# Kernel optimization log

Hardware: AMD Instinct MI355X
Metric: run time of the kernel (lower is better)

The kernel has to match this reference:

```python
import jax, jax.numpy as jnp
import numpy as np

NUM_STATION = 20
NUM_HEADS = 8
INPUT_DIM = 128
KEY_DIM = 16          # = val_dim = embed_dim // num_heads
EMBED_DIM = 128
NORM = 1.0 / np.sqrt(KEY_DIM).astype(np.float32)


def setup_inputs() -> dict:
    key = jax.random.key(0)
    ks = jax.random.split(key, 10)
    B, N, D = 32, 1024, INPUT_DIM
    q = jax.random.normal(ks[0], (B, N, D), jnp.float32)
    h = jax.random.normal(ks[1], (B, N, D), jnp.float32)
    stdv_k = 1.0 / np.sqrt(KEY_DIM)      # torch init: uniform(-1/sqrt(last_dim), ...)
    stdv_e = 1.0 / np.sqrt(EMBED_DIM)
    def U(k, shape, s):
        return jax.random.uniform(k, shape, jnp.float32, -s, s)
    pshape = (NUM_HEADS, INPUT_DIM, KEY_DIM)
    return {
        "q": q,
        "h": h,
        "W_query_custom": U(ks[2], pshape, stdv_k),
        "W_query_custom_1": U(ks[3], pshape, stdv_k),
        "W_key_custom": U(ks[4], pshape, stdv_k),
        "W_val_custom": U(ks[5], pshape, stdv_k),
        "W_query_charge_1": U(ks[6], pshape, stdv_k),
        "W_key_charge": U(ks[7], pshape, stdv_k),
        "W_val_charge": U(ks[8], pshape, stdv_k),
        "W_out": U(ks[9], (NUM_HEADS, KEY_DIM, EMBED_DIM), stdv_e),
    }


def reference(q, h, W_query_custom, W_query_custom_1, W_key_custom, W_val_custom,
              W_query_charge_1, W_key_charge, W_val_charge, W_out):
    S = NUM_STATION + 1                      # depot + stations
    h_st, h_tk = h[:, :S], h[:, S:]          # [B,S,D], [B,T,D]
    q_st, q_tk = q[:, :S], q[:, S:]

    proj = lambda x, W: jnp.einsum('bnd,hdk->hbnk', x, W)

    K_c = proj(h_tk, W_key_custom)           # [H,B,T,K]
    V_c = proj(h_tk, W_val_custom)
    K_s = proj(h_st, W_key_charge)           # [H,B,S,K]
    V_s = proj(h_st, W_val_charge)

    # task -> task attention (queries via W_query_custom_1)
    Q_tt = proj(q_tk, W_query_custom_1)
    A_tt = jax.nn.softmax(NORM * jnp.einsum('hbqk,hbtk->hbqt', Q_tt, K_c), axis=-1)
    heads_t = jnp.einsum('hbqt,hbtk->hbqk', A_tt, V_c)

    # task -> station attention (queries via W_query_custom)
    Q_ts = proj(q_tk, W_query_custom)
    A_ts = jax.nn.softmax(NORM * jnp.einsum('hbqk,hbsk->hbqs', Q_ts, K_s), axis=-1)
    heads_t = heads_t + jnp.einsum('hbqs,hbsk->hbqk', A_ts, V_s)

    # station -> task attention (queries via W_query_charge_1)
    Q_st = proj(q_st, W_query_charge_1)
    A_st = jax.nn.softmax(NORM * jnp.einsum('hbqk,hbtk->hbqt', Q_st, K_c), axis=-1)
    heads_s = jnp.einsum('hbqt,hbtk->hbqk', A_st, V_c)

    heads = jnp.concatenate([heads_s, heads_t], axis=2)   # [H,B,N,K]
    out = jnp.einsum('hbnk,hke->bne', heads, W_out)        # [B,N,E]
    return out
```

## Files before the change

### kernel.cpp

```cpp
#include <hip/hip_runtime.h>

typedef __bf16 bf16x8 __attribute__((ext_vector_type(8)));
typedef float f32x4 __attribute__((ext_vector_type(4)));
typedef float f32x16 __attribute__((ext_vector_type(16)));
typedef unsigned int uint32;
typedef unsigned short u16;

#define NST 21
#define TOK 1003
#define SCL 0.3606737602222409f

union U4B { uint4 u; bf16x8 b; };

__device__ __forceinline__ uint32 pkbf(float a, float b) {
  uint32 ua = __float_as_uint(a), ub = __float_as_uint(b);
  ua += 0x7fffu + ((ua >> 16) & 1u);
  ub += 0x7fffu + ((ub >> 16) & 1u);
  return (ua >> 16) | (ub & 0xffff0000u);
}
__device__ __forceinline__ u16 bf1(float a) {
  uint32 u = __float_as_uint(a);
  u += 0x7fffu + ((u >> 16) & 1u);
  return (u16)(u >> 16);
}
__device__ __forceinline__ uint32 pkperm(float lo, float hi) {
  return __builtin_amdgcn_perm(__float_as_uint(hi), __float_as_uint(lo), 0x07060302u);
}
__device__ __forceinline__ void plswap(uint32& a, uint32& b) {
#if __has_builtin(__builtin_amdgcn_permlane32_swap)
  typedef unsigned int uu2 __attribute__((ext_vector_type(2)));
  uu2 r = __builtin_amdgcn_permlane32_swap(a, b, false, false);
  a = r.x; b = r.y;
#else
  asm volatile("v_permlane32_swap_b32 %0, %1" : "+v"(a), "+v"(b));
#endif
}

__global__ __launch_bounds__(256) void prep(
    const float* __restrict__ q, const float* __restrict__ hx,
    const float* __restrict__ W0, const float* __restrict__ W1,
    const float* __restrict__ W2, const float* __restrict__ W3,
    const float* __restrict__ W4, const float* __restrict__ Wqst,
    const float* __restrict__ Wks, const float* __restrict__ Wvs,
    u16* __restrict__ WtAll, u16* __restrict__ Qm,
    u16* __restrict__ Ks, u16* __restrict__ Vs) {
  int bid = blockIdx.x, tid = threadIdx.x;
  __shared__ float xq2[2][128], xh2[2][128];
  if (bid < 40) {
    int w = bid >> 3, seg = bid & 7;
    const float* W = (w == 0) ? W0 : (w == 1) ? W1 : (w == 2) ? W2
                     : (w == 3) ? W3 : W4;
    u16* dst = WtAll + w * 16384;
#pragma unroll
    for (int it = 0; it < 8; ++it) {
      int i = seg * 2048 + it * 256 + tid;
      int inner = i & 127, outer = i >> 7;
      float v;
      if (w < 4) {
        int h = outer >> 4, k = outer & 15;
        v = W[h * 2048 + inner * 16 + k];
      } else {
        v = W[inner * 128 + outer];
      }
      dst[outer * 128 + inner] = bf1(v);
    }
  } else {
    int t2 = bid - 40;
    int sub = tid >> 7, col = tid & 127;
    int hh = col >> 4, k = col & 15;
    int bs2 = t2 * 2 + sub;
    int b2 = bs2 >> 5, s = bs2 & 31;
    if (s < NST) {
      xq2[sub][col] = q[(size_t)(b2 * 1024 + s) * 128 + col];
      xh2[sub][col] = hx[(size_t)(b2 * 1024 + s) * 128 + col];
    }
    __syncthreads();
    if (s < NST) {
      const float* Wq = Wqst + hh * 2048 + k;
      const float* Wk = Wks + hh * 2048 + k;
      const float* Wv = Wvs + hh * 2048 + k;
      float dq = 0.f, dk_ = 0.f, dv = 0.f;
#pragma unroll 8
      for (int d = 0; d < 128; ++d) {
        float xq = xq2[sub][d], xh = xh2[sub][d];
        dq = fmaf(xq, Wq[d * 16], dq);
        dk_ = fmaf(xh, Wk[d * 16], dk_);
        dv = fmaf(xh, Wv[d * 16], dv);
      }
      Qm[(((size_t)hh * 32 + b2) * 1024 + s) * 16 + k] = bf1(dq * SCL);
      Ks[(((size_t)hh * 32 + b2) * 32 + s) * 16 + k] = bf1(dk_);
      Vs[(((size_t)hh * 32 + b2) * 16 + k) * 32 + s] = bf1(dv);
    } else {
      Ks[(((size_t)hh * 32 + b2) * 32 + s) * 16 + k] = 0;
      Vs[(((size_t)hh * 32 + b2) * 16 + k) * 32 + s] = 0;
    }
  }
}

__global__ __launch_bounds__(256) void proj_pair(
    const float* __restrict__ q, const float* __restrict__ hx,
    const u16* __restrict__ WtAll, u16* __restrict__ Qm,
    u16* __restrict__ Qts, u16* __restrict__ Kc, u16* __restrict__ Vc) {
  __shared__ u16 Wl[128 * 136];
  int pg = blockIdx.x >> 9, mb = blockIdx.x & 511;
  int m0 = mb * 64;
  const float* A = pg ? hx : q;
  int tid = threadIdx.x;
  int wave = tid >> 6, lane = tid & 63;
  int quad = lane >> 4, l15 = lane & 15;
  int mrow = m0 + wave * 16 + l15;

  U4B af[4];
#pragma unroll
  for (int dk = 0; dk < 4; ++dk) {
    const float* Af = A + (size_t)mrow * 128 + dk * 32 + quad * 8;
    float4 a = *(const float4*)Af;
    float4 b = *(const float4*)(Af + 4);
    af[dk].u = make_uint4(pkbf(a.x, a.y), pkbf(a.z, a.w),
                          pkbf(b.x, b.y), pkbf(b.z, b.w));
  }

  int gbase = m0 + wave * 16 + quad * 4;
  int bb = gbase >> 10, n0 = gbase & 1023;

#pragma unroll
  for (int s = 0; s < 2; ++s) {
    int mode = pg * 2 + s;
    const u16* WtG = WtAll + mode * 16384;
    if (s) __syncthreads();
#pragma unroll
    for (int r = 0; r < 8; ++r) {
      int i = r * 256 + tid;
      int e = i >> 4, j = i & 15;
      *(uint4*)&Wl[e * 136 + j * 8] = *(const uint4*)(WtG + e * 128 + j * 8);
    }
    __syncthreads();

    f32x4 c[8];
#pragma unroll
    for (int nt = 0; nt < 8; ++nt)
#pragma unroll
      for (int r = 0; r < 4; ++r) c[nt][r] = 0.f;
#pragma unroll
    for (int dk = 0; dk < 4; ++dk)
#pragma unroll
      for (int nt = 0; nt < 8; ++nt) {
        U4B bg;
        bg.u = *(const uint4*)&Wl[(nt * 16 + l15) * 136 + dk * 32 + quad * 8];
        c[nt] = __builtin_amdgcn_mfma_f32_16x16x32_bf16(af[dk].b, bg.b, c[nt], 0, 0, 0);
      }

    if (mode == 0) {
#pragma unroll
      for (int nt = 0; nt < 8; ++nt)
#pragma unroll
        for (int r = 0; r < 4; ++r) {
          int n = n0 + r;
          if (n < NST) continue;
          Qm[(((size_t)nt * 32 + bb) * 1024 + n) * 16 + l15] = bf1(c[nt][r] * SCL);
        }
    } else if (mode == 1) {
#pragma unroll
      for (int nt = 0; nt < 8; ++nt)
#pragma unroll
        for (int r = 0; r < 4; ++r)
          Qts[(((size_t)nt * 32 + bb) * 1024 + n0 + r) * 16 + l15] =
              bf1(c[nt][r] * SCL);
    } else if (mode == 2) {
#pragma unroll
      for (int nt = 0; nt < 8; ++nt)
#pragma unroll
        for (int r = 0; r < 4; ++r)
          Kc[(((size_t)nt * 32 + bb) * 1024 + n0 + r) * 16 + l15] = bf1(c[nt][r]);
    } else {
#pragma unroll
      for (int nt = 0; nt < 8; ++nt) {
        uint2 w2 = make_uint2(pkbf(c[nt][0], c[nt][1]), pkbf(c[nt][2], c[nt][3]));
        *(uint2*)(Vc + (((size_t)nt * 32 + bb) * 16 + l15) * 1024 + n0) = w2;
      }
    }
  }
}

__global__ __launch_bounds__(256) void outproj(
    const u16* __restrict__ heads, const u16* __restrict__ WtAll,
    float* __restrict__ out) {
  __shared__ u16 Wl[128 * 136];
  const u16* WtG = WtAll + 4 * 16384;
  int tid = threadIdx.x;
#pragma unroll
  for (int r = 0; r < 8; ++r) {
    int i = r * 256 + tid;
    int e = i >> 4, j = i & 15;
    *(uint4*)&Wl[e * 136 + j * 8] = *(const uint4*)(WtG + e * 128 + j * 8);
  }
  __syncthreads();
  int wave = tid >> 6, lane = tid & 63;
  int quad = lane >> 4, l15 = lane & 15;
  int m0 = blockIdx.x * 64;
  int mrow = m0 + wave * 16 + l15;

  f32x4 c[8];
#pragma unroll
  for (int nt = 0; nt < 8; ++nt)
#pragma unroll
    for (int r = 0; r < 4; ++r) c[nt][r] = 0.f;
#pragma unroll
  for (int dk = 0; dk < 4; ++dk) {
    U4B af;
    af.u = *(const uint4*)(heads + (size_t)mrow * 128 + dk * 32 + quad * 8);
#pragma unroll
    for (int nt = 0; nt < 8; ++nt) {
      U4B bg;
      bg.u = *(const uint4*)&Wl[(nt * 16 + l15) * 136 + dk * 32 + quad * 8];
      c[nt] = __builtin_amdgcn_mfma_f32_16x16x32_bf16(af.b, bg.b, c[nt], 0, 0, 0);
    }
  }
  int gbase = m0 + wave * 16 + quad * 4;
#pragma unroll
  for (int nt = 0; nt < 8; ++nt)
#pragma unroll
    for (int r = 0; r < 4; ++r)
      out[(size_t)(gbase + r) * 128 + nt * 16 + l15] = c[nt][r];
}

__global__ __launch_bounds__(256, 8) void attn_main(
    const u16* __restrict__ Qm, const u16* __restrict__ Qts,
    const u16* __restrict__ Kc, const u16* __restrict__ Vc,
    const u16* __restrict__ Ks, const u16* __restrict__ Vs,
    u16* __restrict__ heads) {
  int bx = blockIdx.x;
  int hb = bx & 255, qc = bx >> 8;
  int h = hb >> 5, b = hb & 31;
  int tid = threadIdx.x;
  int wave = tid >> 6, lane = tid & 63;
  int l5 = lane >> 5, l31 = lane & 31;

  __shared__ u16 Kl[128 * 26];
  __shared__ u16 Vl[32 * 140];
  __shared__ u16 KsL[32 * 26];
  __shared__ u16 VsL[32 * 44];

  const u16* Qbase = Qm + ((size_t)(h * 32 + b)) * 16384;
  const u16* QtsB = Qts + ((size_t)(h * 32 + b)) * 16384;
  const u16* Kbase = Kc + ((size_t)(h * 32 + b)) * 16384;
  const u16* Vbase = Vc + ((size_t)(h * 32 + b)) * 16384;
  const u16* KsB = Ks + (size_t)(h * 32 + b) * 512;
  const u16* VsB = Vs + (size_t)(h * 32 + b) * 512;

  uint4 ones4 = make_uint4(0x3F803F80u, 0x3F803F80u, 0x3F803F80u, 0x3F803F80u);

  if (tid < 64) {
    int key = tid >> 1, half = tid & 1;
    *(uint4*)&KsL[key * 26 + half * 8] = *(const uint4*)(KsB + key * 16 + half * 8);
  } else if (tid < 128) {
    int t = tid - 64;
    int d = t >> 2, kg = t & 3;
    *(uint4*)&VsL[d * 44 + kg * 8] = *(const uint4*)(VsB + d * 32 + kg * 8);
  } else if (tid < 192) {
    int t = tid - 128;
    *(uint4*)&VsL[(16 + (t >> 2)) * 44 + (t & 3) * 8] = ones4;
  }
  *(uint4*)&Vl[(16 + (tid >> 4)) * 140 + (tid & 15) * 8] = ones4;

  int skey = tid >> 1, shalf = tid & 1;
  int sd = tid >> 4, skg = tid & 15;
  uint4 kpre = *(const uint4*)(Kbase + (size_t)skey * 16 + shalf * 8);
  uint4 vpre = *(const uint4*)(Vbase + (size_t)sd * 1024 + skg * 8);

  int qw0 = qc * 128 + wave * 32;
  int qrow = qw0 + l31;

  f32x16 zero16;
#pragma unroll
  for (int i = 0; i < 16; ++i) zero16[i] = 0.f;

  U4B qf;
  qf.u = *(const uint4*)(QtsB + (size_t)qrow * 16 + l5 * 8);
  __syncthreads();
  float contrib[8];
  {
    U4B af;
    af.u = *(const uint4*)&KsL[l31 * 26 + l5 * 8];
    f32x16 c0 =
        __builtin_amdgcn_mfma_f32_32x32x16_bf16(af.b, qf.b, zero16, 0, 0, 0);
    uint32 w[8];
#pragma unroll
    for (int g = 0; g < 4; ++g) {
      float p0 = __builtin_amdgcn_exp2f(c0[4 * g + 0]);
      float p1 = __builtin_amdgcn_exp2f(c0[4 * g + 1]);
      float p2 = __builtin_amdgcn_exp2f(c0[4 * g + 2]);
      float p3 = __builtin_amdgcn_exp2f(c0[4 * g + 3]);
      int kb0 = 8 * g + 4 * l5;
      p0 = (kb0 + 0 >= NST) ? 0.f : p0;
      p1 = (kb0 + 1 >= NST) ? 0.f : p1;
      p2 = (kb0 + 2 >= NST) ? 0.f : p2;
      p3 = (kb0 + 3 >= NST) ? 0.f : p3;
      w[2 * g] = pkperm(p0, p1);
      w[2 * g + 1] = pkperm(p2, p3);
    }
    plswap(w[0], w[2]); plswap(w[1], w[3]);
    plswap(w[4], w[6]); plswap(w[5], w[7]);
    U4B b1, b2, a1, a2;
    b1.u = make_uint4(w[0], w[1], w[2], w[3]);
    b2.u = make_uint4(w[4], w[5], w[6], w[7]);
    a1.u = *(const uint4*)&VsL[l31 * 44 + l5 * 8];
    a2.u = *(const uint4*)&VsL[l31 * 44 + 16 + l5 * 8];
    f32x16 acc2 =
        __builtin_amdgcn_mfma_f32_32x32x16_bf16(a1.b, b1.b, zero16, 0, 0, 0);
    acc2 = __builtin_amdgcn_mfma_f32_32x32x16_bf16(a2.b, b2.b, acc2, 0, 0, 0);
    float rla2 = __builtin_amdgcn_rcpf(acc2[8]);
#pragma unroll
    for (int r = 0; r < 8; ++r) contrib[r] = acc2[r] * rla2;
  }

  qf.u = *(const uint4*)(Qbase + (size_t)qrow * 16 + l5 * 8);
  f32x16 acc;
#pragma unroll
  for (int i = 0; i < 16; ++i) acc[i] = 0.f;

#pragma unroll 1
  for (int kb = 0; kb < 8; ++kb) {
    __syncthreads();
    *(uint4*)&Kl[skey * 26 + shalf * 8] = kpre;
    *(uint4*)&Vl[sd * 140 + skg * 8] = vpre;
    if (kb < 7) {
      int j0n = (kb + 1) * 128;
      kpre = *(const uint4*)(Kbase + (size_t)(j0n + skey) * 16 + shalf * 8);
      vpre = *(const uint4*)(Vbase + (size_t)sd * 1024 + j0n + skg * 8);
    }
    __syncthreads();
#pragma unroll 1
    for (int kt = 0; kt < 4; ++kt) {
      int key0 = kt * 32;
      U4B af;
      af.u = *(const uint4*)&Kl[(key0 + l31) * 26 + l5 * 8];
      f32x16 c0 =
          __builtin_amdgcn_mfma_f32_32x32x16_bf16(af.b, qf.b, zero16, 0, 0, 0);
      bool masked = (kb == 0) && (kt == 0);
      uint32 w[8];
#pragma unroll
      for (int g = 0; g < 4; ++g) {
        float p0 = __builtin_amdgcn_exp2f(c0[4 * g + 0]);
        float p1 = __builtin_amdgcn_exp2f(c0[4 * g + 1]);
        float p2 = __builtin_amdgcn_exp2f(c0[4 * g + 2]);
        float p3 = __builtin_amdgcn_exp2f(c0[4 * g + 3]);
        if (masked) {
          int kb0 = 8 * g + 4 * l5;
          p0 = (kb0 + 0 < NST) ? 0.f : p0;
          p1 = (kb0 + 1 < NST) ? 0.f : p1;
          p2 = (kb0 + 2 < NST) ? 0.f : p2;
          p3 = (kb0 + 3 < NST) ? 0.f : p3;
        }
        w[2 * g] = pkperm(p0, p1);
        w[2 * g + 1] = pkperm(p2, p3);
      }
      plswap(w[0], w[2]); plswap(w[1], w[3]);
      plswap(w[4], w[6]); plswap(w[5], w[7]);
      U4B b1, b2, a1, a2;
      b1.u = make_uint4(w[0], w[1], w[2], w[3]);
      b2.u = make_uint4(w[4], w[5], w[6], w[7]);
      a1.u = *(const uint4*)&Vl[l31 * 140 + key0 + l5 * 8];
      a2.u = *(const uint4*)&Vl[l31 * 140 + key0 + 16 + l5 * 8];
      acc = __builtin_amdgcn_mfma_f32_32x32x16_bf16(a1.b, b1.b, acc, 0, 0, 0);
      acc = __builtin_amdgcn_mfma_f32_32x32x16_bf16(a2.b, b2.b, acc, 0, 0, 0);
    }
  }

  {
    float rla = __builtin_amdgcn_rcpf(acc[8]);
    bool tok = (qrow >= NST);
    float v0 = acc[0] * rla + (tok ? contrib[0] : 0.f);
    float v1 = acc[1] * rla + (tok ? contrib[1] : 0.f);
    float v2 = acc[2] * rla + (tok ? contrib[2] : 0.f);
    float v3 = acc[3] * rla + (tok ? contrib[3] : 0.f);
    float v4 = acc[4] * rla + (tok ? contrib[4] : 0.f);
    float v5 = acc[5] * rla + (tok ? contrib[5] : 0.f);
    float v6 = acc[6] * rla + (tok ? contrib[6] : 0.f);
    float v7 = acc[7] * rla + (tok ? contrib[7] : 0.f);
    u16* hrow = heads + ((size_t)b * 1024 + qrow) * 128 + h * 16;
    *(uint2*)(hrow + 4 * l5) = make_uint2(pkbf(v0, v1), pkbf(v2, v3));
    *(uint2*)(hrow + 8 + 4 * l5) = make_uint2(pkbf(v4, v5), pkbf(v6, v7));
  }
}

extern "C" void kernel_launch(void* const* d_in, const int* in_sizes, int n_in,
                              void* d_out, int out_size, void* d_ws,
                              size_t ws_size, hipStream_t stream) {
  (void)in_sizes; (void)n_in; (void)out_size; (void)ws_size;
  const float* q     = (const float*)d_in[0];
  const float* hx    = (const float*)d_in[1];
  const float* W_qts = (const float*)d_in[2];
  const float* W_qtt = (const float*)d_in[3];
  const float* W_kc  = (const float*)d_in[4];
  const float* W_vc  = (const float*)d_in[5];
  const float* W_qst = (const float*)d_in[6];
  const float* W_ks  = (const float*)d_in[7];
  const float* W_vs  = (const float*)d_in[8];
  const float* W_out = (const float*)d_in[9];

  char* ws = (char*)d_ws;
  u16* heads = (u16*)(ws + 0);
  u16* Qm    = (u16*)(ws + 16777216);
  u16* Qts   = (u16*)(ws + 25165824);
  u16* Kc    = (u16*)(ws + 33554432);
  u16* Vc    = (u16*)(ws + 41943040);
  u16* Ks    = (u16*)(ws + 50331648);
  u16* Vs    = (u16*)(ws + 50593792);
  u16* WtAll = (u16*)(ws + 50855936);

  hipLaunchKernelGGL(prep, dim3(552), dim3(256), 0, stream,
                     q, hx, W_qtt, W_qts, W_kc, W_vc, W_out, W_qst, W_ks, W_vs,
                     WtAll, Qm, Ks, Vs);
  hipLaunchKernelGGL(proj_pair, dim3(1024), dim3(256), 0, stream,
                     q, hx, WtAll, Qm, Qts, Kc, Vc);
  hipLaunchKernelGGL(attn_main, dim3(2048), dim3(256), 0, stream,
                     Qm, Qts, Kc, Vc, Ks, Vs, heads);
  hipLaunchKernelGGL(outproj, dim3(512), dim3(256), 0, stream,
                     heads, WtAll, (float*)d_out);
}
```

Before: 160.2 us.

## Pipeline QK MFMA one tile ahead and vectorize projection/output stores

```diff
diff --git a/kernel.cpp b/kernel.cpp
--- a/kernel.cpp
+++ b/kernel.cpp
@@ -122,6 +122,8 @@
 
   int gbase = m0 + wave * 16 + quad * 4;
   int bb = gbase >> 10, n0 = gbase & 1023;
+  int token = mrow;
+  int bb2 = token >> 10, tn = token & 1023;
 
 #pragma unroll
   for (int s = 0; s < 2; ++s) {
@@ -147,36 +149,28 @@
       for (int nt = 0; nt < 8; ++nt) {
         U4B bg;
         bg.u = *(const uint4*)&Wl[(nt * 16 + l15) * 136 + dk * 32 + quad * 8];
-        c[nt] = __builtin_amdgcn_mfma_f32_16x16x32_bf16(af[dk].b, bg.b, c[nt], 0, 0, 0);
-      }
-
-    if (mode == 0) {
-#pragma unroll
-      for (int nt = 0; nt < 8; ++nt)
-#pragma unroll
-        for (int r = 0; r < 4; ++r) {
-          int n = n0 + r;
-          if (n < NST) continue;
-          Qm[(((size_t)nt * 32 + bb) * 1024 + n) * 16 + l15] = bf1(c[nt][r] * SCL);
-        }
-    } else if (mode == 1) {
-#pragma unroll
-      for (int nt = 0; nt < 8; ++nt)
-#pragma unroll
-        for (int r = 0; r < 4; ++r)
-          Qts[(((size_t)nt * 32 + bb) * 1024 + n0 + r) * 16 + l15] =
-              bf1(c[nt][r] * SCL);
-    } else if (mode == 2) {
-#pragma unroll
-      for (int nt = 0; nt < 8; ++nt)
-#pragma unroll
-        for (int r = 0; r < 4; ++r)
-          Kc[(((size_t)nt * 32 + bb) * 1024 + n0 + r) * 16 + l15] = bf1(c[nt][r]);
-    } else {
+        if (mode == 3)
+          c[nt] = __builtin_amdgcn_mfma_f32_16x16x32_bf16(af[dk].b, bg.b, c[nt], 0, 0, 0);
+        else
+          c[nt] = __builtin_amdgcn_mfma_f32_16x16x32_bf16(bg.b, af[dk].b, c[nt], 0, 0, 0);
+      }
+
+    if (mode == 3) {
 #pragma unroll
       for (int nt = 0; nt < 8; ++nt) {
         uint2 w2 = make_uint2(pkbf(c[nt][0], c[nt][1]), pkbf(c[nt][2], c[nt][3]));
         *(uint2*)(Vc + (((size_t)nt * 32 + bb) * 16 + l15) * 1024 + n0) = w2;
+      }
+    } else {
+      float scale = (mode <= 1) ? SCL : 1.0f;
+      u16* dstp = (mode == 0) ? Qm : (mode == 1) ? Qts : Kc;
+      if (mode != 0 || tn >= NST) {
+#pragma unroll
+        for (int nt = 0; nt < 8; ++nt) {
+          uint2 w2 = make_uint2(pkbf(c[nt][0] * scale, c[nt][1] * scale),
+                                pkbf(c[nt][2] * scale, c[nt][3] * scale));
+          *(uint2*)(dstp + (((size_t)nt * 32 + bb2) * 1024 + tn) * 16 + quad * 4) = w2;
+        }
       }
     }
   }
@@ -213,18 +207,15 @@
     for (int nt = 0; nt < 8; ++nt) {
       U4B bg;
       bg.u = *(const uint4*)&Wl[(nt * 16 + l15) * 136 + dk * 32 + quad * 8];
-      c[nt] = __builtin_amdgcn_mfma_f32_16x16x32_bf16(af.b, bg.b, c[nt], 0, 0, 0);
-    }
-  }
-  int gbase = m0 + wave * 16 + quad * 4;
+      c[nt] = __builtin_amdgcn_mfma_f32_16x16x32_bf16(bg.b, af.b, c[nt], 0, 0, 0);
+    }
+  }
 #pragma unroll
   for (int nt = 0; nt < 8; ++nt)
-#pragma unroll
-    for (int r = 0; r < 4; ++r)
-      out[(size_t)(gbase + r) * 128 + nt * 16 + l15] = c[nt][r];
-}
-
-__global__ __launch_bounds__(256, 8) void attn_main(
+    *(f32x4*)(out + (size_t)mrow * 128 + nt * 16 + quad * 4) = c[nt];
+}
+
+__global__ __launch_bounds__(256, 6) void attn_main(
     const u16* __restrict__ Qm, const u16* __restrict__ Qts,
     const u16* __restrict__ Kc, const u16* __restrict__ Vc,
     const u16* __restrict__ Ks, const u16* __restrict__ Vs,
@@ -330,13 +321,20 @@
       vpre = *(const uint4*)(Vbase + (size_t)sd * 1024 + j0n + skg * 8);
     }
     __syncthreads();
-#pragma unroll 1
+
+    U4B af0;
+    af0.u = *(const uint4*)&Kl[l31 * 26 + l5 * 8];
+    f32x16 c0 =
+        __builtin_amdgcn_mfma_f32_32x32x16_bf16(af0.b, qf.b, zero16, 0, 0, 0);
+#pragma unroll
     for (int kt = 0; kt < 4; ++kt) {
+      f32x16 cn;
+      if (kt < 3) {
+        U4B afn;
+        afn.u = *(const uint4*)&Kl[((kt + 1) * 32 + l31) * 26 + l5 * 8];
+        cn = __builtin_amdgcn_mfma_f32_32x32x16_bf16(afn.b, qf.b, zero16, 0, 0, 0);
+      }
       int key0 = kt * 32;
-      U4B af;
-      af.u = *(const uint4*)&Kl[(key0 + l31) * 26 + l5 * 8];
-      f32x16 c0 =
-          __builtin_amdgcn_mfma_f32_32x32x16_bf16(af.b, qf.b, zero16, 0, 0, 0);
       bool masked = (kb == 0) && (kt == 0);
       uint32 w[8];
 #pragma unroll
@@ -364,6 +362,7 @@
       a2.u = *(const uint4*)&Vl[l31 * 140 + key0 + 16 + l5 * 8];
       acc = __builtin_amdgcn_mfma_f32_32x32x16_bf16(a1.b, b1.b, acc, 0, 0, 0);
       acc = __builtin_amdgcn_mfma_f32_32x32x16_bf16(a2.b, b2.b, acc, 0, 0, 0);
+      if (kt < 3) c0 = cn;
     }
   }
 
```

Result: slower. 164.9 us (+2.9%).
